# Optimization experiments

Hardware: AMD Instinct MI355X
Metric: run time of the kernel (lower is better)

The kernel has to match this reference:

```python
import jax, jax.numpy as jnp
import numpy as np

B, T, E, H, D = 2, 2048, 1024, 16, 64
ROPE_BASE = 10000.0


def project(x, k):
    # Lift to Lorentz hyperboloid with curvature magnitude K=exp(k): <lx,lx>_L = -K
    K = jnp.exp(k)
    x0 = jnp.sqrt(K + jnp.sum(x * x, axis=-1, keepdims=True))
    return jnp.concatenate([x0, x], axis=-1)


def layer_norm(x, w, b, eps=1e-5):
    m = jnp.mean(x, axis=-1, keepdims=True)
    v = jnp.mean((x - m) ** 2, axis=-1, keepdims=True)
    return (x - m) * jax.lax.rsqrt(v + eps) * w + b


def setup_inputs() -> dict:
    key = jax.random.key(0)
    ks = jax.random.split(key, 8)
    s = 0.02
    return dict(
        x=jax.random.normal(ks[0], (B, T, E), jnp.float32),
        block_curvature=jnp.asarray(1.0, jnp.float32),
        mlp_curvature=jnp.asarray(1.0, jnp.float32),
        attn_curvatures=jnp.ones((1, H, 1, 1), jnp.float32),
        w_qkv=jax.random.normal(ks[1], (E + 1, 3 * E), jnp.float32) * s,
        w_attn_proj=jax.random.normal(ks[2], ((D + 1) * H, E), jnp.float32) * s,
        b_attn_proj=jnp.zeros((E,), jnp.float32),
        w_mlp_expand=jax.random.normal(ks[3], (E + 1, 4 * E + 3), jnp.float32) * s,
        b_mlp_expand=jnp.zeros((4 * E + 3,), jnp.float32),
        w_mlp_shrink=jax.random.normal(ks[4], (4 * (E + 1), E), jnp.float32) * s,
        b_mlp_shrink=jnp.zeros((E,), jnp.float32),
        ln_w=jnp.ones((E,), jnp.float32),
        ln_b=jnp.zeros((E,), jnp.float32),
    )


def _block(x, block_curvature, mlp_curvature, attn_curvatures, w_qkv,
           w_attn_proj, b_attn_proj, w_mlp_expand, b_mlp_expand,
           w_mlp_shrink, b_mlp_shrink, ln_w, ln_b):
    Bq, Tq = x.shape[0], x.shape[1]
    lx = project(x, block_curvature)  # (B,T,E+1)

    def block_norm(l):
        return project(layer_norm(l[..., 1:], ln_w, ln_b), block_curvature)

    def skip(l, f):  # hyperbolic skip: add space parts, re-lift
        return project(l[..., 1:] + f[..., 1:], block_curvature)

    def attn(l):
        qkv = l @ w_qkv  # (B,T,3E)
        q, k, v = jnp.split(qkv, 3, axis=-1)
        q = q.reshape(Bq, Tq, H, D)
        k = k.reshape(Bq, Tq, H, D)
        v = v.reshape(Bq, Tq, H, D)
        half = D // 2
        inv_freq = 1.0 / (ROPE_BASE ** (jnp.arange(0, D, 2, dtype=jnp.float32) / D))
        freqs = jnp.arange(Tq, dtype=jnp.float32)[:, None] * inv_freq[None, :]
        cos = jnp.cos(freqs)[None, :, None, :]  # (1,T,1,D/2)
        sin = jnp.sin(freqs)[None, :, None, :]

        def rope(t):
            t1, t2 = t[..., :half], t[..., half:]
            return jnp.concatenate([t1 * cos + t2 * sin, -t1 * sin + t2 * cos], axis=-1)

        q = rope(q).transpose(0, 2, 1, 3)  # (B,H,T,D)
        k = rope(k).transpose(0, 2, 1, 3)
        v = v.transpose(0, 2, 1, 3)
        K = jnp.exp(attn_curvatures)  # (1,H,1,1) per-head curvature
        qt = jnp.sqrt(K + jnp.sum(q * q, axis=-1, keepdims=True))  # time coord (B,H,T,1)
        kt = jnp.sqrt(K + jnp.sum(k * k, axis=-1, keepdims=True))
        lv = project(v, attn_curvatures)  # (B,H,T,D+1)
        # Lorentz inner product without materializing (B,H,T,T,D+1)
        inner = jnp.einsum('bhtd,bhsd->bhts', q, k) - qt * jnp.swapaxes(kt, -1, -2)
        ratio = jnp.maximum(-inner / K, 1.0 + 1e-7)
        dis = jnp.sqrt(K) * jnp.arccosh(ratio)  # (B,H,T,T)
        causal = jnp.tril(jnp.ones((Tq, Tq), dtype=bool))
        w = jnp.where(causal, -dis, -jnp.inf)  # neg_dis attention weight + causal bias
        aw = jax.nn.softmax(w, axis=-1)
        o = jnp.einsum('bhts,bhse->bhte', aw, lv)  # (B,H,T,D+1)
        lnorm2 = o[..., :1] ** 2 - jnp.sum(o[..., 1:] ** 2, axis=-1, keepdims=True)
        hn = jnp.sqrt(jnp.maximum(lnorm2, 1e-12))  # Lorentz norm
        o = o * jnp.sqrt(K) / hn  # renormalize back onto hyperboloid
        o = o.transpose(0, 2, 1, 3).reshape(Bq, Tq, H * (D + 1))
        return project(o @ w_attn_proj + b_attn_proj, block_curvature)

    def mlp(l):
        h = project(l @ w_mlp_expand + b_mlp_expand, mlp_curvature)[..., 1:]  # (B,T,4E+3)
        h = jax.nn.gelu(h, approximate=False)
        h = project(h, mlp_curvature)  # (B,T,4(E+1))
        return project(h @ w_mlp_shrink + b_mlp_shrink, block_curvature)

    lx = skip(lx, attn(block_norm(lx)))
    lx = skip(lx, mlp(block_norm(lx)))
    return lx


def reference(x, block_curvature, mlp_curvature, attn_curvatures, w_qkv,
              w_attn_proj, b_attn_proj, w_mlp_expand, b_mlp_expand,
              w_mlp_shrink, b_mlp_shrink, ln_w, ln_b):
    return _block(x, block_curvature, mlp_curvature, attn_curvatures, w_qkv,
                  w_attn_proj, b_attn_proj, w_mlp_expand, b_mlp_expand,
                  w_mlp_shrink, b_mlp_shrink, ln_w, ln_b)
```

## Files before the change

### kernel.cpp

```cpp
#include <hip/hip_runtime.h>
#include <math.h>

#define MM   4096
#define TT   2048
#define HH   16

typedef __bf16 bf16x8 __attribute__((ext_vector_type(8)));
typedef float f32x4 __attribute__((ext_vector_type(4)));

__device__ __forceinline__ void g2l16(const void* g, void* l) {
    __builtin_amdgcn_global_load_lds(
        (__attribute__((address_space(1))) void*)g,
        (__attribute__((address_space(3))) void*)l, 16, 0, 0);
}

#if __has_builtin(__builtin_amdgcn_exp2f)
__device__ __forceinline__ float fexp2(float x) { return __builtin_amdgcn_exp2f(x); }
#else
__device__ __forceinline__ float fexp2(float x) { return exp2f(x); }
#endif
#if __has_builtin(__builtin_amdgcn_logf)
__device__ __forceinline__ float flog2(float x) { return __builtin_amdgcn_logf(x); }
#else
__device__ __forceinline__ float flog2(float x) { return log2f(x); }
#endif
#if __has_builtin(__builtin_amdgcn_sqrtf)
__device__ __forceinline__ float fsqrt_(float x) { return __builtin_amdgcn_sqrtf(x); }
#else
__device__ __forceinline__ float fsqrt_(float x) { return sqrtf(x); }
#endif
#if __has_builtin(__builtin_amdgcn_rcpf)
__device__ __forceinline__ float frcp_(float x) { return __builtin_amdgcn_rcpf(x); }
#else
__device__ __forceinline__ float frcp_(float x) { return 1.0f / x; }
#endif
#if __has_builtin(__builtin_amdgcn_rsqf)
__device__ __forceinline__ float frsq_(float x) { return __builtin_amdgcn_rsqf(x); }
#else
__device__ __forceinline__ float frsq_(float x) { return rsqrtf(x); }
#endif

__device__ __forceinline__ float gelu_f(float x) {
    float u = 0.7978845608028654f * fmaf(0.044715f * x, x * x, x);
    u = fminf(fmaxf(u, -15.f), 15.f);
    float t = fexp2(-2.885390081777927f * u);
    return 0.5f * x * (1.f + (1.f - t) * frcp_(1.f + t));
}

__device__ __forceinline__ float blockSum256(float v, volatile float* sb) {
    int lane = threadIdx.x & 63, w = threadIdx.x >> 6;
#pragma unroll
    for (int o = 32; o; o >>= 1) v += __shfl_xor(v, o);
    if (lane == 0) sb[w] = v;
    __syncthreads();
    v = sb[0] + sb[1] + sb[2] + sb[3];
    __syncthreads();
    return v;
}

__global__ __launch_bounds__(256) void block_norm_bf_k(
    const float* __restrict__ in, int ld,
    __bf16* __restrict__ out, int ldo,
    const float* __restrict__ lw, const float* __restrict__ lb,
    const float* __restrict__ curv)
{
    int row = blockIdx.x;
    const float* x = in + (size_t)row * ld;
    __bf16* o = out + (size_t)row * ldo;
    __shared__ float sb[4];
    int tid = threadIdx.x;
    float v[4]; float s1 = 0.f, s2 = 0.f;
#pragma unroll
    for (int r = 0; r < 4; r++) {
        float t = x[tid + 256 * r];
        v[r] = t; s1 += t; s2 += t * t;
    }
    s1 = blockSum256(s1, sb);
    s2 = blockSum256(s2, sb);
    float mean = s1 * (1.f / 1024.f);
    float var  = s2 * (1.f / 1024.f) - mean * mean;
    float rs = rsqrtf(var + 1e-5f);
    float y[4]; float ssq = 0.f;
#pragma unroll
    for (int r = 0; r < 4; r++) {
        int i = tid + 256 * r;
        float t = (v[r] - mean) * rs * lw[i] + lb[i];
        y[r] = t; ssq += t * t;
    }
    ssq = blockSum256(ssq, sb);
#pragma unroll
    for (int r = 0; r < 4; r++) o[1 + tid + 256 * r] = (__bf16)y[r];
    if (tid == 0) o[0] = (__bf16)sqrtf(expf(*curv) + ssq);
    if (tid < ldo - 1025) o[1025 + tid] = (__bf16)0.f;
}

__global__ __launch_bounds__(256) void row_x0_k(
    float* __restrict__ buf, int stride, int n, const float* __restrict__ curv)
{
    int row = blockIdx.x;
    float* base = buf + (size_t)row * stride;
    __shared__ float sb[4];
    float s = 0.f;
    for (int i = threadIdx.x; i < n; i += 256) { float t = base[1 + i]; s += t * t; }
    s = blockSum256(s, sb);
    if (threadIdx.x == 0) base[0] = sqrtf(expf(*curv) + s);
}

__global__ __launch_bounds__(256) void row_x0_tail_k(
    __bf16* __restrict__ h,
    const __bf16* __restrict__ ln,
    const __bf16* __restrict__ Bt,
    const float* __restrict__ bias,
    const float* __restrict__ curv)
{
    int row = blockIdx.x;
    __bf16* base = h + (size_t)row * 4224;
    const __bf16* lnr = ln + (size_t)row * 1088;
    const __bf16* B0 = Bt + (size_t)4096 * 1088;
    const __bf16* B1 = Bt + (size_t)4097 * 1088;
    const __bf16* B2 = Bt + (size_t)4098 * 1088;
    __shared__ float sb[4];
    float d0 = 0.f, d1 = 0.f, d2 = 0.f;
    for (int i = threadIdx.x; i < 1088; i += 256) {
        float a = (float)lnr[i];
        d0 += a * (float)B0[i];
        d1 += a * (float)B1[i];
        d2 += a * (float)B2[i];
    }
    d0 = blockSum256(d0, sb);
    d1 = blockSum256(d1, sb);
    d2 = blockSum256(d2, sb);
    float t3[3] = {d0 + bias[4096], d1 + bias[4097], d2 + bias[4098]};
    float ssq_t = 0.f;
#pragma unroll
    for (int j = 0; j < 3; j++) {
        float v = gelu_f(t3[j]);
        t3[j] = v; ssq_t += v * v;
    }
    if (threadIdx.x == 0) {
        base[1 + 4096] = (__bf16)t3[0];
        base[1 + 4097] = (__bf16)t3[1];
        base[1 + 4098] = (__bf16)t3[2];
    }
    float s = 0.f;
    for (int i = threadIdx.x; i < 4096; i += 256) { float t = (float)base[1 + i]; s += t * t; }
    s = blockSum256(s, sb) + ssq_t;
    if (threadIdx.x == 0) base[0] = (__bf16)sqrtf(expf(*curv) + s);
    if (threadIdx.x < 124) base[4100 + threadIdx.x] = (__bf16)0.f;
}

__global__ __launch_bounds__(256) void wt_k(
    const float* __restrict__ W, int K, int N,
    __bf16* __restrict__ Wt, int Kp)
{
    __shared__ float s[32][33];
    int tx = threadIdx.x & 31, ty = threadIdx.x >> 5;
    int k0 = blockIdx.x * 32, n0 = blockIdx.y * 32;
#pragma unroll
    for (int r = 0; r < 4; r++) {
        int k = k0 + ty + 8 * r, n = n0 + tx;
        s[ty + 8 * r][tx] = (k < K && n < N) ? W[(size_t)k * N + n] : 0.f;
    }
    __syncthreads();
#pragma unroll
    for (int r = 0; r < 4; r++) {
        int n = n0 + ty + 8 * r, k = k0 + tx;
        if (n < N) Wt[(size_t)n * Kp + k] = (__bf16)s[tx][ty + 8 * r];
    }
}

template<bool BIAS, bool GELU, bool OUTBF>
__global__ __launch_bounds__(512, 2) void mgemm256_k(
    const __bf16* __restrict__ A, int lda,
    const __bf16* __restrict__ Bt, int ldb, int NB,
    const float* __restrict__ bias,
    void* __restrict__ Cout, int ldc,
    int N, int Kp)
{
    __shared__ __bf16 sAB[65536];
    const int tid = threadIdx.x;
    const int w = tid >> 6, lane = tid & 63;
    const int wm = w >> 2, wn = w & 3;
    const int lr = lane & 15, lq = lane >> 4;

    const int lin = blockIdx.y * gridDim.x + blockIdx.x;
    const int xcd = lin & 7, loc = lin >> 3;
    const int LN = gridDim.x >> 1, LM = gridDim.y >> 2;
    const int mt = (xcd >> 1) * LM + loc / LN;
    const int nt = (xcd & 1) * LN + loc % LN;
    const int m0 = mt * 256, n0 = nt * 256;

    const int rr  = tid >> 3;
    const int csw = ((tid & 7) ^ (rr & 7)) << 3;
    const __bf16* gA[4]; const __bf16* gB[4];
#pragma unroll
    for (int c = 0; c < 4; c++) {
        gA[c] = A + (size_t)(m0 + c * 64 + rr) * lda + csw;
        int rb = n0 + c * 64 + rr; rb = (rb < NB) ? rb : (NB - 1);
        gB[c] = Bt + (size_t)rb * ldb + csw;
    }
    __bf16* lA = sAB + (w << 9);
    __bf16* lB = sAB + 32768 + (w << 9);

    const int off0 = (lq * 8) ^ ((lr & 7) << 3);
    const int off1 = off0 ^ 32;
    const int arow = wm * 128 + lr;
    const int brow = wn * 64 + lr;

    f32x4 zero = {0.f, 0.f, 0.f, 0.f};
    f32x4 acc[8][4];
#pragma unroll
    for (int i = 0; i < 8; i++)
#pragma unroll
        for (int j = 0; j < 4; j++) acc[i][j] = zero;

#pragma unroll
    for (int c = 0; c < 4; c++) {
        g2l16(gA[c], lA + c * 4096);
        g2l16(gB[c], lB + c * 4096);
    }
    asm volatile("s_waitcnt vmcnt(0)" ::: "memory");
    __builtin_amdgcn_s_barrier();

    const int NT = Kp >> 6;
    for (int kt = 0; kt < NT; ++kt) {
        const int cur = kt & 1;
        const __bf16* pA = sAB + cur * 16384;
        const __bf16* pB = sAB + 32768 + cur * 16384;
        bf16x8 af[4][2], bfr[4][2];

        if (kt + 1 < NT) {
            const int ko = (kt + 1) << 6;
            __bf16* dA = lA + (cur ^ 1) * 16384;
            __bf16* dB = lB + (cur ^ 1) * 16384;
#pragma unroll
            for (int c = 0; c < 4; c++) {
                g2l16(gA[c] + ko, dA + c * 4096);
                g2l16(gB[c] + ko, dB + c * 4096);
            }
        }
#pragma unroll
        for (int i = 0; i < 4; i++) {
            const __bf16* r = pA + (arow + i * 16) * 64;
            af[i][0] = *(const bf16x8*)(r + off0);
            af[i][1] = *(const bf16x8*)(r + off1);
        }
#pragma unroll
        for (int j = 0; j < 2; j++) {
            const __bf16* r = pB + (brow + j * 16) * 64;
            bfr[j][0] = *(const bf16x8*)(r + off0);
            bfr[j][1] = *(const bf16x8*)(r + off1);
        }
        __builtin_amdgcn_s_barrier();
        __builtin_amdgcn_s_setprio(1);
#pragma unroll
        for (int ks = 0; ks < 2; ks++)
#pragma unroll
            for (int i = 0; i < 4; i++)
#pragma unroll
                for (int j = 0; j < 2; j++)
                    acc[i][j] = __builtin_amdgcn_mfma_f32_16x16x32_bf16(af[i][ks], bfr[j][ks], acc[i][j], 0, 0, 0);
        __builtin_amdgcn_s_setprio(0);
        __builtin_amdgcn_s_barrier();

#pragma unroll
        for (int j = 2; j < 4; j++) {
            const __bf16* r = pB + (brow + j * 16) * 64;
            bfr[j][0] = *(const bf16x8*)(r + off0);
            bfr[j][1] = *(const bf16x8*)(r + off1);
        }
        __builtin_amdgcn_s_barrier();
        __builtin_amdgcn_s_setprio(1);
#pragma unroll
        for (int ks = 0; ks < 2; ks++)
#pragma unroll
            for (int i = 0; i < 4; i++)
#pragma unroll
                for (int j = 2; j < 4; j++)
                    acc[i][j] = __builtin_amdgcn_mfma_f32_16x16x32_bf16(af[i][ks], bfr[j][ks], acc[i][j], 0, 0, 0);
        __builtin_amdgcn_s_setprio(0);
        __builtin_amdgcn_s_barrier();

#pragma unroll
        for (int i = 0; i < 4; i++) {
            const __bf16* r = pA + (arow + 64 + i * 16) * 64;
            af[i][0] = *(const bf16x8*)(r + off0);
            af[i][1] = *(const bf16x8*)(r + off1);
        }
        __builtin_amdgcn_s_barrier();
        __builtin_amdgcn_s_setprio(1);
#pragma unroll
        for (int ks = 0; ks < 2; ks++)
#pragma unroll
            for (int i = 0; i < 4; i++)
#pragma unroll
                for (int j = 0; j < 2; j++)
                    acc[4 + i][j] = __builtin_amdgcn_mfma_f32_16x16x32_bf16(af[i][ks], bfr[j][ks], acc[4 + i][j], 0, 0, 0);
        __builtin_amdgcn_s_setprio(0);
        __builtin_amdgcn_s_barrier();

        __builtin_amdgcn_s_setprio(1);
#pragma unroll
        for (int ks = 0; ks < 2; ks++)
#pragma unroll
            for (int i = 0; i < 4; i++)
#pragma unroll
                for (int j = 2; j < 4; j++)
                    acc[4 + i][j] = __builtin_amdgcn_mfma_f32_16x16x32_bf16(af[i][ks], bfr[j][ks], acc[4 + i][j], 0, 0, 0);
        __builtin_amdgcn_s_setprio(0);
        asm volatile("s_waitcnt vmcnt(0) lgkmcnt(0)" ::: "memory");
        __builtin_amdgcn_s_barrier();
    }

#pragma unroll
    for (int j = 0; j < 4; j++) {
        const int n = n0 + wn * 64 + j * 16 + lr;
        if (n < N) {
            const float bv = BIAS ? bias[n] : 0.f;
#pragma unroll
            for (int i = 0; i < 8; i++) {
#pragma unroll
                for (int r = 0; r < 4; r++) {
                    const int m = m0 + wm * 128 + i * 16 + lq * 4 + r;
                    float v = acc[i][j][r] + bv;
                    if (GELU) v = gelu_f(v);
                    if (OUTBF) ((__bf16*)Cout)[(size_t)m * ldc + n] = (__bf16)v;
                    else       ((float*)Cout)[(size_t)m * ldc + n] = v;
                }
            }
        }
    }
}

template<bool BIAS, bool GELU, bool SKIP>
__global__ __launch_bounds__(256, 2) void mgemm128_k(
    const __bf16* __restrict__ A, int lda,
    const __bf16* __restrict__ Bt, int ldb,
    const float* __restrict__ bias,
    const float* __restrict__ skip, int ldskip,
    float* __restrict__ Cout, int ldc,
    int N, int Kp)
{
    __shared__ __bf16 sAB[32768];
    const int tid = threadIdx.x;
    const int w = tid >> 6, lane = tid & 63;
    const int wm = w >> 1, wn = w & 1;
    const int lr = lane & 15, lq = lane >> 4;

    const int bid = blockIdx.x;
    const int cpx = gridDim.x >> 3;
    const int swz = (bid & 7) * cpx + (bid >> 3);
    const int m0 = (swz >> 3) * 128, n0 = (swz & 7) * 128;

    const int rr  = tid >> 3;
    const int csw = ((tid & 7) ^ (rr & 7)) << 3;
    const __bf16* gA[4]; const __bf16* gB[4];
#pragma unroll
    for (int c = 0; c < 4; c++) {
        gA[c] = A + (size_t)(m0 + c * 32 + rr) * lda + csw;
        gB[c] = Bt + (size_t)(n0 + c * 32 + rr) * ldb + csw;
    }
    __bf16* lA = sAB + (w << 9);
    __bf16* lB = sAB + 16384 + (w << 9);

    const int off0 = (lq * 8) ^ ((lr & 7) << 3);
    const int off1 = off0 ^ 32;
    const int arow = wm * 64 + lr;
    const int brow = wn * 64 + lr;

    f32x4 zero = {0.f, 0.f, 0.f, 0.f};
    f32x4 acc[4][4];
#pragma unroll
    for (int i = 0; i < 4; i++)
#pragma unroll
        for (int j = 0; j < 4; j++) acc[i][j] = zero;

#pragma unroll
    for (int c = 0; c < 4; c++) {
        g2l16(gA[c], lA + c * 2048);
        g2l16(gB[c], lB + c * 2048);
    }
    asm volatile("s_waitcnt vmcnt(0)" ::: "memory");
    __builtin_amdgcn_s_barrier();

    const int NT = Kp >> 6;
    for (int kt = 0; kt < NT; ++kt) {
        const int cur = kt & 1;
        const __bf16* pA = sAB + cur * 8192;
        const __bf16* pB = sAB + 16384 + cur * 8192;
        bf16x8 af[4][2], bfr[4][2];

        if (kt + 1 < NT) {
            const int ko = (kt + 1) << 6;
            __bf16* dA = lA + (cur ^ 1) * 8192;
            __bf16* dB = lB + (cur ^ 1) * 8192;
#pragma unroll
            for (int c = 0; c < 4; c++) {
                g2l16(gA[c] + ko, dA + c * 2048);
                g2l16(gB[c] + ko, dB + c * 2048);
            }
        }
#pragma unroll
        for (int i = 0; i < 4; i++) {
            const __bf16* r = pA + (arow + i * 16) * 64;
            af[i][0] = *(const bf16x8*)(r + off0);
            af[i][1] = *(const bf16x8*)(r + off1);
        }
#pragma unroll
        for (int j = 0; j < 2; j++) {
            const __bf16* r = pB + (brow + j * 16) * 64;
            bfr[j][0] = *(const bf16x8*)(r + off0);
            bfr[j][1] = *(const bf16x8*)(r + off1);
        }
        __builtin_amdgcn_s_barrier();
        __builtin_amdgcn_s_setprio(1);
#pragma unroll
        for (int ks = 0; ks < 2; ks++)
#pragma unroll
            for (int i = 0; i < 4; i++)
#pragma unroll
                for (int j = 0; j < 2; j++)
                    acc[i][j] = __builtin_amdgcn_mfma_f32_16x16x32_bf16(af[i][ks], bfr[j][ks], acc[i][j], 0, 0, 0);
        __builtin_amdgcn_s_setprio(0);
        __builtin_amdgcn_s_barrier();

#pragma unroll
        for (int j = 2; j < 4; j++) {
            const __bf16* r = pB + (brow + j * 16) * 64;
            bfr[j][0] = *(const bf16x8*)(r + off0);
            bfr[j][1] = *(const bf16x8*)(r + off1);
        }
        __builtin_amdgcn_s_barrier();
        __builtin_amdgcn_s_setprio(1);
#pragma unroll
        for (int ks = 0; ks < 2; ks++)
#pragma unroll
            for (int i = 0; i < 4; i++)
#pragma unroll
                for (int j = 2; j < 4; j++)
                    acc[i][j] = __builtin_amdgcn_mfma_f32_16x16x32_bf16(af[i][ks], bfr[j][ks], acc[i][j], 0, 0, 0);
        __builtin_amdgcn_s_setprio(0);
        asm volatile("s_waitcnt vmcnt(0) lgkmcnt(0)" ::: "memory");
        __builtin_amdgcn_s_barrier();
    }

#pragma unroll
    for (int j = 0; j < 4; j++) {
        const int n = n0 + wn * 64 + j * 16 + lr;
        if (n < N) {
            const float bv = BIAS ? bias[n] : 0.f;
#pragma unroll
            for (int i = 0; i < 4; i++) {
#pragma unroll
                for (int r = 0; r < 4; r++) {
                    const int m = m0 + wm * 64 + i * 16 + lq * 4 + r;
                    float v = acc[i][j][r] + bv;
                    if (GELU) v = gelu_f(v);
                    if (SKIP) v += skip[(size_t)m * ldskip + n];
                    Cout[(size_t)m * ldc + n] = v;
                }
            }
        }
    }
}

__global__ __launch_bounds__(256) void rope_k(
    float* __restrict__ QKV, const float* __restrict__ curv,
    float* __restrict__ qt, float* __restrict__ kt,
    __bf16* __restrict__ Kb, __bf16* __restrict__ Obf)
{
    int row = blockIdx.x;
    int b = row >> 11, t = row & (TT - 1);
    int wv = threadIdx.x >> 6, d = threadIdx.x & 63;
    int j = d & 31;
    float fr = (float)t * powf(10000.0f, -(float)(2 * j) / 64.0f);
    float cv = cosf(fr), sv = sinf(fr);
    float sgn = (d < 32) ? sv : -sv;
    for (int h = wv; h < HH; h += 4) {
        float Kh = expf(curv[h]);
        float* base = QKV + (size_t)row * 3072 + h * 64;
        float q = base[d], k = base[1024 + d];
        float qp = __shfl_xor(q, 32);
        float kp = __shfl_xor(k, 32);
        float qr = q * cv + qp * sgn;
        float kr = k * cv + kp * sgn;
        base[d] = qr;
        size_t oidx = ((size_t)(b * HH + h) * TT + t);
        Kb[oidx * 64 + d] = (__bf16)kr;
        float sq = qr * qr, sk = kr * kr;
#pragma unroll
        for (int o = 32; o; o >>= 1) {
            sq += __shfl_xor(sq, o);
            sk += __shfl_xor(sk, o);
        }
        if (d == 0) {
            qt[oidx] = sqrtf(Kh + sq);
            kt[oidx] = sqrtf(Kh + sk);
        }
    }
    if (threadIdx.x < 48) Obf[(size_t)row * 1088 + 1040 + threadIdx.x] = (__bf16)0.f;
}

__global__ __launch_bounds__(256) void vtrans_k(
    const float* __restrict__ QKV, const float* __restrict__ curv,
    __bf16* __restrict__ Vtb, float* __restrict__ vt)
{
    __shared__ float sT[64 * 65];
    int bh = blockIdx.y; int h = bh & (HH - 1); int b = bh >> 4;
    int t0 = blockIdx.x * 64;
    int tid = threadIdx.x, w = tid >> 6, lane = tid & 63;
    float Kh = expf(curv[h]);
    const float* vbase = QKV + (size_t)(b * TT + t0) * 3072 + 2048 + h * 64;
#pragma unroll 4
    for (int i = 0; i < 16; i++) {
        int tr = w * 16 + i;
        float v = vbase[(size_t)tr * 3072 + lane];
        sT[lane * 65 + tr] = v;
        float s = v * v;
#pragma unroll
        for (int o = 32; o; o >>= 1) s += __shfl_xor(s, o);
        if (lane == 0) vt[(size_t)bh * TT + t0 + tr] = sqrtf(Kh + s);
    }
    __syncthreads();
    int d = tid >> 2, seg = tid & 3;
    const float* r = &sT[d * 65 + seg * 16];
    bf16x8 o0, o1;
#pragma unroll
    for (int i = 0; i < 8; i++) { o0[i] = (__bf16)r[i]; o1[i] = (__bf16)r[8 + i]; }
    __bf16* dst = Vtb + ((size_t)bh * 64 + d) * TT + t0 + seg * 16;
    *(bf16x8*)dst = o0;
    *(bf16x8*)(dst + 8) = o1;
}

__global__ __launch_bounds__(256, 4) void flash_k(
    const float* __restrict__ QKV,
    const __bf16* __restrict__ Kb, const __bf16* __restrict__ Vtb,
    const float* __restrict__ qt, const float* __restrict__ kt,
    const float* __restrict__ vt,
    const float* __restrict__ curv,
    __bf16* __restrict__ O)
{
    __shared__ __bf16 sK[4096];
    __shared__ __bf16 sVt[4096];
    __shared__ __bf16 sP[4 * 16 * 72];
    __shared__ float skt[64], svt[64];

    int bh = blockIdx.x; int h = bh & (HH - 1); int b = bh >> 4;
    int pi = blockIdx.y;
    float Kh = expf(curv[h]);
    float sqKh = sqrtf(Kh), msqK = -sqKh, invKh = 1.0f / Kh;
    const float* tok = QKV + (size_t)b * TT * 3072 + h * 64;
    const char* KbB = (const char*)Kb + (size_t)bh * TT * 128;
    const char* VtB = (const char*)Vtb + (size_t)bh * 64 * (TT * 2);
    const float* qtp = qt + (size_t)bh * TT;
    const float* ktp = kt + (size_t)bh * TT;
    const float* vtp = vt + (size_t)bh * TT;

    int tid = threadIdx.x;
    int w = tid >> 6, lane = tid & 63;
    int m = lane & 15, quad = lane >> 4;
    int qA = pi * 32, qB = (63 - pi) * 32;
    int myBase = (w < 2) ? (qA + 16 * w) : (qB + 16 * (w - 2));
    int myJmax = (myBase + 15) >> 6;
    int blockJmax = (qB + 31) >> 6;
    __bf16* sPw = &sP[w * 16 * 72];

    bf16x8 qhi[2], qlo[2];
    {
        const float* qrow = tok + (size_t)(myBase + m) * 3072;
#pragma unroll
        for (int ks = 0; ks < 2; ks++) {
            const float* s = qrow + quad * 8 + 32 * ks;
            float4 f0 = *(const float4*)s;
            float4 f1 = *(const float4*)(s + 4);
            float fa[8] = {f0.x, f0.y, f0.z, f0.w, f1.x, f1.y, f1.z, f1.w};
#pragma unroll
            for (int jj = 0; jj < 8; jj++) {
                __bf16 hv = (__bf16)fa[jj];
                qhi[ks][jj] = hv;
                qlo[ks][jj] = (__bf16)(fa[jj] - (float)hv);
            }
        }
    }
    float qtv[4]; int qg[4];
#pragma unroll
    for (int r = 0; r < 4; r++) { qg[r] = myBase + quad * 4 + r; qtv[r] = qtp[qg[r]]; }

    f32x4 zero = {0.f, 0.f, 0.f, 0.f};
    f32x4 accO[4];
#pragma unroll
    for (int nt = 0; nt < 4; nt++) accO[nt] = zero;
    float lsumr[4] = {}, o0r[4] = {};

    char* sKb  = (char*)sK  + w * 1024;
    char* sVb  = (char*)sVt + w * 1024;

    for (int j = 0; j <= blockJmax; ++j) {
        int sb = j << 6;
        __syncthreads();
        {
            const char* kg = KbB + (size_t)(sb + lane) * 128 + w * 16;
            g2l16(kg,      sKb);
            g2l16(kg + 64, sKb + 4096);
            const char* vg = VtB + (size_t)lane * (TT * 2) + sb * 2 + w * 16;
            g2l16(vg,      sVb);
            g2l16(vg + 64, sVb + 4096);
        }
        if (tid < 64) skt[tid] = ktp[sb + tid];
        else if (tid < 128) svt[tid - 64] = vtp[sb + tid - 64];
        __syncthreads();

        if (j > myJmax) continue;

        f32x4 accS[4];
#pragma unroll
        for (int nt = 0; nt < 4; nt++) accS[nt] = zero;
#pragma unroll
        for (int nt = 0; nt < 4; nt++) {
#pragma unroll
            for (int ksp = 0; ksp < 2; ksp++) {
                bf16x8 bk = *(const bf16x8*)&sK[((ksp * 4 + quad) * 64 + nt * 16 + m) * 8];
                accS[nt] = __builtin_amdgcn_mfma_f32_16x16x32_bf16(qhi[ksp], bk, accS[nt], 0, 0, 0);
                accS[nt] = __builtin_amdgcn_mfma_f32_16x16x32_bf16(qlo[ksp], bk, accS[nt], 0, 0, 0);
            }
        }
#pragma unroll
        for (int nt = 0; nt < 4; nt++) {
            int col = nt * 16 + m;
            int sglob = sb + col;
            float ktv = skt[col], vtv = svt[col];
#pragma unroll
            for (int r = 0; r < 4; r++) {
                float dot = accS[nt][r];
                float rdiff = fmaf(qtv[r], ktv, -dot);
                float ratio = fmaxf(rdiff * invKh, 1.0f + 1e-7f);
                float y = ratio + fsqrt_(fmaf(ratio, ratio, -1.0f));
                float pv = fexp2(msqK * flog2(y));
                float p = (sglob <= qg[r]) ? pv : 0.0f;
                lsumr[r] += p;
                o0r[r] = fmaf(p, vtv, o0r[r]);
                sPw[(quad * 4 + r) * 72 + col] = (__bf16)p;
            }
        }
        __asm__ volatile("s_waitcnt lgkmcnt(0)" ::: "memory");
#pragma unroll
        for (int ksp = 0; ksp < 2; ksp++) {
            bf16x8 aP = *(const bf16x8*)&sPw[m * 72 + ksp * 32 + quad * 8];
#pragma unroll
            for (int nt = 0; nt < 4; nt++) {
                bf16x8 bV = *(const bf16x8*)&sVt[((ksp * 4 + quad) * 64 + nt * 16 + m) * 8];
                accO[nt] = __builtin_amdgcn_mfma_f32_16x16x32_bf16(aP, bV, accO[nt], 0, 0, 0);
            }
        }
    }

#pragma unroll
    for (int r = 0; r < 4; r++) {
#pragma unroll
        for (int off = 1; off < 16; off <<= 1) {
            lsumr[r] += __shfl_xor(lsumr[r], off);
            o0r[r]   += __shfl_xor(o0r[r], off);
        }
    }
#pragma unroll
    for (int r = 0; r < 4; r++) {
        float inv = frcp_(lsumr[r]);
        float o0f = o0r[r] * inv;
        float ov[4]; float part = 0.f;
#pragma unroll
        for (int nt = 0; nt < 4; nt++) { float t = accO[nt][r] * inv; ov[nt] = t; part += t * t; }
        part += __shfl_xor(part, 1);
        part += __shfl_xor(part, 2);
        part += __shfl_xor(part, 4);
        part += __shfl_xor(part, 8);
        float scale = sqKh * frsq_(fmaxf(o0f * o0f - part, 1e-12f));
        size_t orow = (size_t)(b * TT + qg[r]) * 1088 + h * 65;
        if (m == 0) O[orow] = (__bf16)(o0f * scale);
#pragma unroll
        for (int nt = 0; nt < 4; nt++) O[orow + 1 + nt * 16 + m] = (__bf16)(ov[nt] * scale);
    }
}

extern "C" void kernel_launch(void* const* d_in, const int* in_sizes, int n_in,
                              void* d_out, int out_size, void* d_ws, size_t ws_size,
                              hipStream_t stream) {
    const float* x    = (const float*)d_in[0];
    const float* bc   = (const float*)d_in[1];
    const float* mc   = (const float*)d_in[2];
    const float* ac   = (const float*)d_in[3];
    const float* w_qkv = (const float*)d_in[4];
    const float* w_ap  = (const float*)d_in[5];
    const float* b_ap  = (const float*)d_in[6];
    const float* w_me  = (const float*)d_in[7];
    const float* b_me  = (const float*)d_in[8];
    const float* w_ms  = (const float*)d_in[9];
    const float* b_ms  = (const float*)d_in[10];
    const float* lnw  = (const float*)d_in[11];
    const float* lnb  = (const float*)d_in[12];
    float* out = (float*)d_out;
    float* ws  = (float*)d_ws;

    float* R      = ws;
    float* qkvbuf = R;
    float* X2     = R;
    __bf16* h_bf  = (__bf16*)(R + 4194304);
    float* p      = R + 12845056;
    __bf16* ln_bf = (__bf16*)p;  p += 2228224;
    __bf16* o_bf  = (__bf16*)p;  p += 2228224;
    __bf16* qkvT  = (__bf16*)p;  p += 1671168;
    __bf16* apT   = (__bf16*)p;  p += 557056;
    float*  meT_f = p;           p += 2229856;
    float*  msT_f = p;           p += 2162688;
    float* Qt = p;               p += 2 * HH * TT;
    float* Kt = p;               p += 2 * HH * TT;
    float* Vt = p;
    __bf16* meT = (__bf16*)meT_f;
    __bf16* msT = (__bf16*)msT_f;
    __bf16* Kb  = (__bf16*)meT_f;
    __bf16* Vtb = (__bf16*)msT_f;

    wt_k<<<dim3(34, 96),  256, 0, stream>>>(w_qkv, 1025, 3072, qkvT, 1088);
    wt_k<<<dim3(34, 32),  256, 0, stream>>>(w_ap,  1040, 1024, apT,  1088);

    block_norm_bf_k<<<MM, 256, 0, stream>>>(x, 1024, ln_bf, 1088, lnw, lnb, bc);
    mgemm256_k<false, false, false><<<dim3(12, 16), 512, 0, stream>>>(
        ln_bf, 1088, qkvT, 1088, 3072, nullptr, qkvbuf, 3072, 3072, 1088);
    rope_k<<<MM, 256, 0, stream>>>(qkvbuf, ac, Qt, Kt, Kb, o_bf);
    vtrans_k<<<dim3(32, 32), 256, 0, stream>>>(qkvbuf, ac, Vtb, Vt);
    flash_k<<<dim3(2 * HH, 32), 256, 0, stream>>>(qkvbuf, Kb, Vtb, Qt, Kt, Vt, ac, o_bf);
    wt_k<<<dim3(34, 129), 256, 0, stream>>>(w_me,  1025, 4099, meT, 1088);
    wt_k<<<dim3(132, 32), 256, 0, stream>>>(w_ms,  4100, 1024, msT, 4224);
    mgemm128_k<true, false, true><<<dim3(256), 256, 0, stream>>>(
        o_bf, 1088, apT, 1088, b_ap, x, 1024, X2, 1024, 1024, 1088);
    block_norm_bf_k<<<MM, 256, 0, stream>>>(X2, 1024, ln_bf, 1088, lnw, lnb, bc);
    mgemm256_k<true, true, true><<<dim3(16, 16), 512, 0, stream>>>(
        ln_bf, 1088, meT, 1088, 4099, b_me, (void*)(h_bf + 1), 4224, 4099, 1088);
    row_x0_tail_k<<<MM, 256, 0, stream>>>(h_bf, ln_bf, meT, b_me, mc);
    mgemm128_k<true, false, true><<<dim3(256), 256, 0, stream>>>(
        h_bf, 4224, msT, 4224, b_ms, X2, 1024, out + 1, 1025, 1024, 4224);
    row_x0_k<<<MM, 256, 0, stream>>>(out, 1025, 1024, bc);
}
```

Baseline: 453.5 us.

## Double-buffer K/V tiles in flash kernel and schedule contiguous query tiles

The attention kernel now keeps two LDS buffers for the K, V-transpose and per-key time-coordinate tiles. The next key tile is prefetched while the current one is being computed, and one barrier per iteration replaces the previous two. Each block now owns 64 contiguous query rows, with the longest causal ranges launched first, instead of pairing a short and a long 32-row tile per block. Occupancy is lowered to 3 blocks per CU to fit the doubled shared memory. The per-warp causal skip inside a block goes away, and the change depends on the heavy-first ordering for load balance.

```diff
diff --git a/kernel.cpp b/kernel.cpp
--- a/kernel.cpp
+++ b/kernel.cpp
@@ -532,7 +532,7 @@
     *(bf16x8*)(dst + 8) = o1;
 }
 
-__global__ __launch_bounds__(256, 4) void flash_k(
+__global__ __launch_bounds__(256, 3) void flash_k(
     const float* __restrict__ QKV,
     const __bf16* __restrict__ Kb, const __bf16* __restrict__ Vtb,
     const float* __restrict__ qt, const float* __restrict__ kt,
@@ -540,13 +540,15 @@
     const float* __restrict__ curv,
     __bf16* __restrict__ O)
 {
-    __shared__ __bf16 sK[4096];
-    __shared__ __bf16 sVt[4096];
+    __shared__ __bf16 sK[2][4096];
+    __shared__ __bf16 sVt[2][4096];
     __shared__ __bf16 sP[4 * 16 * 72];
-    __shared__ float skt[64], svt[64];
+    __shared__ float skt[2][64], svt[2][64];
 
     int bh = blockIdx.x; int h = bh & (HH - 1); int b = bh >> 4;
-    int pi = blockIdx.y;
+    int qti = 31 - (int)blockIdx.y;
+    int q0 = qti << 6;
+    int NJ = qti + 1;
     float Kh = expf(curv[h]);
     float sqKh = sqrtf(Kh), msqK = -sqKh, invKh = 1.0f / Kh;
     const float* tok = QKV + (size_t)b * TT * 3072 + h * 64;
@@ -559,10 +561,7 @@
     int tid = threadIdx.x;
     int w = tid >> 6, lane = tid & 63;
     int m = lane & 15, quad = lane >> 4;
-    int qA = pi * 32, qB = (63 - pi) * 32;
-    int myBase = (w < 2) ? (qA + 16 * w) : (qB + 16 * (w - 2));
-    int myJmax = (myBase + 15) >> 6;
-    int blockJmax = (qB + 31) >> 6;
+    int myBase = q0 + 16 * w;
     __bf16* sPw = &sP[w * 16 * 72];
 
     bf16x8 qhi[2], qlo[2];
@@ -592,25 +591,36 @@
     for (int nt = 0; nt < 4; nt++) accO[nt] = zero;
     float lsumr[4] = {}, o0r[4] = {};
 
-    char* sKb  = (char*)sK  + w * 1024;
-    char* sVb  = (char*)sVt + w * 1024;
-
-    for (int j = 0; j <= blockJmax; ++j) {
+    {
+        const char* kg = KbB + (size_t)lane * 128 + w * 16;
+        char* sKb = (char*)&sK[0][0] + w * 1024;
+        g2l16(kg,      sKb);
+        g2l16(kg + 64, sKb + 4096);
+        const char* vg = VtB + (size_t)lane * (TT * 2) + w * 16;
+        char* sVb = (char*)&sVt[0][0] + w * 1024;
+        g2l16(vg,      sVb);
+        g2l16(vg + 64, sVb + 4096);
+    }
+    if (tid < 64) skt[0][tid] = ktp[tid];
+    else if (tid < 128) svt[0][tid - 64] = vtp[tid - 64];
+    __syncthreads();
+
+    for (int j = 0; j < NJ; ++j) {
+        int cur = j & 1;
         int sb = j << 6;
-        __syncthreads();
-        {
-            const char* kg = KbB + (size_t)(sb + lane) * 128 + w * 16;
+        if (j + 1 < NJ) {
+            int sb2 = sb + 64;
+            const char* kg = KbB + (size_t)(sb2 + lane) * 128 + w * 16;
+            char* sKb = (char*)&sK[cur ^ 1][0] + w * 1024;
             g2l16(kg,      sKb);
             g2l16(kg + 64, sKb + 4096);
-            const char* vg = VtB + (size_t)lane * (TT * 2) + sb * 2 + w * 16;
+            const char* vg = VtB + (size_t)lane * (TT * 2) + sb2 * 2 + w * 16;
+            char* sVb = (char*)&sVt[cur ^ 1][0] + w * 1024;
             g2l16(vg,      sVb);
             g2l16(vg + 64, sVb + 4096);
-        }
-        if (tid < 64) skt[tid] = ktp[sb + tid];
-        else if (tid < 128) svt[tid - 64] = vtp[sb + tid - 64];
-        __syncthreads();
-
-        if (j > myJmax) continue;
+            if (tid < 64) skt[cur ^ 1][tid] = ktp[sb2 + tid];
+            else if (tid < 128) svt[cur ^ 1][tid - 64] = vtp[sb2 + tid - 64];
+        }
 
         f32x4 accS[4];
 #pragma unroll
@@ -619,7 +629,7 @@
         for (int nt = 0; nt < 4; nt++) {
 #pragma unroll
             for (int ksp = 0; ksp < 2; ksp++) {
-                bf16x8 bk = *(const bf16x8*)&sK[((ksp * 4 + quad) * 64 + nt * 16 + m) * 8];
+                bf16x8 bk = *(const bf16x8*)&sK[cur][((ksp * 4 + quad) * 64 + nt * 16 + m) * 8];
                 accS[nt] = __builtin_amdgcn_mfma_f32_16x16x32_bf16(qhi[ksp], bk, accS[nt], 0, 0, 0);
                 accS[nt] = __builtin_amdgcn_mfma_f32_16x16x32_bf16(qlo[ksp], bk, accS[nt], 0, 0, 0);
             }
@@ -628,7 +638,7 @@
         for (int nt = 0; nt < 4; nt++) {
             int col = nt * 16 + m;
             int sglob = sb + col;
-            float ktv = skt[col], vtv = svt[col];
+            float ktv = skt[cur][col], vtv = svt[cur][col];
 #pragma unroll
             for (int r = 0; r < 4; r++) {
                 float dot = accS[nt][r];
@@ -648,10 +658,11 @@
             bf16x8 aP = *(const bf16x8*)&sPw[m * 72 + ksp * 32 + quad * 8];
 #pragma unroll
             for (int nt = 0; nt < 4; nt++) {
-                bf16x8 bV = *(const bf16x8*)&sVt[((ksp * 4 + quad) * 64 + nt * 16 + m) * 8];
+                bf16x8 bV = *(const bf16x8*)&sVt[cur][((ksp * 4 + quad) * 64 + nt * 16 + m) * 8];
                 accO[nt] = __builtin_amdgcn_mfma_f32_16x16x32_bf16(aP, bV, accO[nt], 0, 0, 0);
             }
         }
+        __syncthreads();
     }
 
 #pragma unroll
```

Result: faster. 444.4 us (-2.0%).
